# Kernel optimization log

Hardware: AMD Instinct MI355X
Metric: run time of the kernel (lower is better)

Reference implementation:

```python
import jax, jax.numpy as jnp
import numpy as np


def setup_inputs() -> dict:
    key = jax.random.key(0)
    ks = jax.random.split(key, 7)
    B, T, D, H = 32, 512, 512, 512
    return {
        "x": jax.random.normal(ks[0], (B, T, D), dtype=jnp.float32),
        "W_Du": jax.random.normal(ks[1], (D, H), dtype=jnp.float32) * (1.0 / np.sqrt(D)),
        "W_Dr1": jax.random.normal(ks[2], (D, H), dtype=jnp.float32) * (1.0 / np.sqrt(D)),
        "W_Dr2": jax.random.normal(ks[3], (D, H), dtype=jnp.float32) * (1.0 / np.sqrt(D)),
        "b_Du": jax.random.normal(ks[4], (H,), dtype=jnp.float32) * 0.02,
        "b_Dr1": jax.random.normal(ks[5], (H,), dtype=jnp.float32) * 0.02,
        "b_Dr2": jax.random.normal(ks[6], (H,), dtype=jnp.float32) * 0.02,
    }


def reference(x, W_Du, W_Dr1, W_Dr2, b_Du, b_Dr1, b_Dr2):
    # Precompute all per-step projections across time (batched matmuls),
    # then run the strictly sequential gated recurrence with lax.scan.
    r1 = jax.nn.softmax(jnp.einsum('btd,dh->bth', x, W_Dr1) + b_Dr1, axis=-1)  # [B,T,H]
    r2 = jax.nn.softmax(jnp.einsum('btd,dh->bth', x, W_Dr2) + b_Dr2, axis=-1)  # [B,T,H]
    u = jnp.tanh(jnp.einsum('btd,dh->bth', x, W_Du) + b_Du)                     # [B,T,H]

    def step(s, inp):
        r1t, r2t, ut = inp
        s_new = r1t * s + r2t * ut
        return s_new, s_new

    init = jnp.zeros((x.shape[0], W_Du.shape[1]), dtype=x.dtype)
    # time-major for scan: [T,B,H]
    _, ys = jax.lax.scan(
        step, init,
        (jnp.swapaxes(r1, 0, 1), jnp.swapaxes(r2, 0, 1), jnp.swapaxes(u, 0, 1)),
    )
    return jnp.swapaxes(ys, 0, 1)  # [B,T,H]
```

## Files before the change

### kernel.cpp

```cpp
#include <hip/hip_runtime.h>
#include <hip/hip_bf16.h>

#define B_N 32
#define T_N 512
#define D_N 512
#define H_N 512
#define M_N (B_N * T_N)

typedef __attribute__((ext_vector_type(8))) short bf16x8;
typedef __attribute__((ext_vector_type(4))) float f32x4;

__device__ __forceinline__ unsigned short f2bf(float f) {
  unsigned u = __float_as_uint(f);
  u += 0x7FFFu + ((u >> 16) & 1u);
  return (unsigned short)(u >> 16);
}
__device__ __forceinline__ float bf2f(unsigned short h) {
  return __uint_as_float(((unsigned)h) << 16);
}
__device__ __forceinline__ unsigned short f2h(float f) {
  _Float16 h = (_Float16)f;
  return *(unsigned short*)&h;
}
__device__ __forceinline__ float h2f(unsigned short u) {
  _Float16 h = *(_Float16*)&u;
  return (float)h;
}

#define GLOAD16(g, l) __builtin_amdgcn_global_load_lds( \
    (const __attribute__((address_space(1))) void*)(g), \
    (__attribute__((address_space(3))) void*)(l), 16, 0, 0)

__global__ void prep_kernel(const float* __restrict__ x,
                            const float* __restrict__ W0,
                            const float* __restrict__ W1,
                            const float* __restrict__ W2,
                            unsigned short* __restrict__ xb,
                            unsigned short* __restrict__ Wt) {
  int blk = blockIdx.x;
  int tid = threadIdx.x;
  if (blk < 768) {
    __shared__ float tile[32][33];
    int id = blk >> 8;
    int t = blk & 255;
    int kr = (t >> 4) << 5;
    int nc = (t & 15) << 5;
    const float* W = (id == 0) ? W0 : (id == 1) ? W1 : W2;
    unsigned short* Wo = Wt + (size_t)id * (D_N * H_N);
    int tx = tid & 31, ty0 = tid >> 5;
    for (int ty = ty0; ty < 32; ty += 8)
      tile[ty][tx] = W[(size_t)(kr + ty) * H_N + nc + tx];
    __syncthreads();
    for (int ty = ty0; ty < 32; ty += 8)
      Wo[(size_t)(nc + ty) * D_N + kr + tx] = f2bf(tile[tx][ty]);
  } else {
    int b = blk - 768;
    const float4* xv = (const float4*)x;
#pragma unroll
    for (int u = 0; u < 4; ++u) {
      int i = b * 1024 + u * 256 + tid;
      float4 v = xv[i];
      ushort4 o;
      o.x = f2bf(v.x); o.y = f2bf(v.y); o.z = f2bf(v.z); o.w = f2bf(v.w);
      ((ushort4*)xb)[i] = o;
    }
  }
}

__global__ __launch_bounds__(256) void gemm3(
    const unsigned short* __restrict__ xb,
    const unsigned short* __restrict__ Wt,
    const float* __restrict__ bDu,
    const float* __restrict__ bDr1,
    const float* __restrict__ bDr2,
    unsigned short* __restrict__ uP,
    unsigned short* __restrict__ e1P,
    unsigned short* __restrict__ e2P) {
  __shared__ __align__(16) char smem[65536];

  const int tid = threadIdx.x;
  const int lane = tid & 63;
  const int wv = tid >> 6;
  const int wr = wv >> 1;
  const int wc = wv & 1;
  const int g = lane >> 4;
  const int c16 = lane & 15;

  const int m0 = blockIdx.x * 128;
  const int n0 = blockIdx.y * 128;
  const int id = blockIdx.z;
  const unsigned short* Wp = Wt + (size_t)id * (D_N * H_N);

  f32x4 acc[4][4];
#pragma unroll
  for (int mt = 0; mt < 4; ++mt)
#pragma unroll
    for (int nt = 0; nt < 4; ++nt)
      acc[mt][nt] = (f32x4){0.f, 0.f, 0.f, 0.f};

  const int rowoff = tid >> 3;
  const int lsl = ((tid & 7) ^ ((tid >> 3) & 7)) * 8;
  const unsigned short* aSrc = xb + (size_t)(m0 + rowoff) * D_N + lsl;
  const unsigned short* bSrc = Wp + (size_t)(n0 + rowoff) * D_N + lsl;
  const int dstOff = wv * 1024;

  const int h3 = c16 & 7;

#define STAGE(buf, kstep) do {                                           \
    const int k0_ = (kstep) * 64;                                        \
    _Pragma("unroll")                                                    \
    for (int i = 0; i < 4; ++i)                                          \
      GLOAD16(aSrc + (size_t)i * (32 * D_N) + k0_,                       \
              smem + (buf) * 16384 + dstOff + i * 4096);                 \
    _Pragma("unroll")                                                    \
    for (int i = 0; i < 4; ++i)                                          \
      GLOAD16(bSrc + (size_t)i * (32 * D_N) + k0_,                       \
              smem + 32768 + (buf) * 16384 + dstOff + i * 4096);         \
  } while (0)

#define COMPUTE(buf) do {                                                \
    _Pragma("unroll")                                                    \
    for (int kh = 0; kh < 2; ++kh) {                                     \
      const int soff = ((kh * 4 + g) ^ h3) << 4;                         \
      bf16x8 af[4], bb[4];                                               \
      _Pragma("unroll")                                                  \
      for (int mt = 0; mt < 4; ++mt)                                     \
        af[mt] = *(const bf16x8*)(smem + (buf) * 16384 +                 \
                                  (wr * 64 + mt * 16 + c16) * 128 + soff); \
      _Pragma("unroll")                                                  \
      for (int nt = 0; nt < 4; ++nt)                                     \
        bb[nt] = *(const bf16x8*)(smem + 32768 + (buf) * 16384 +         \
                                  (wc * 64 + nt * 16 + c16) * 128 + soff); \
      _Pragma("unroll")                                                  \
      for (int mt = 0; mt < 4; ++mt)                                     \
        _Pragma("unroll")                                                \
        for (int nt = 0; nt < 4; ++nt)                                   \
          acc[mt][nt] = __builtin_amdgcn_mfma_f32_16x16x32_bf16(         \
              af[mt], bb[nt], acc[mt][nt], 0, 0, 0);                     \
    }                                                                    \
  } while (0)

#define WAIT8 asm volatile("s_waitcnt vmcnt(8)" ::: "memory")

  STAGE(0, 0);
#pragma unroll 1
  for (int i = 0; i < 3; ++i) {
    STAGE(1, 2 * i + 1);
    WAIT8;
    __syncthreads();
    COMPUTE(0);
    __syncthreads();
    STAGE(0, 2 * i + 2);
    WAIT8;
    __syncthreads();
    COMPUTE(1);
    __syncthreads();
  }
  STAGE(1, 7);
  WAIT8;
  __syncthreads();
  COMPUTE(0);
  __syncthreads();
  asm volatile("s_waitcnt vmcnt(0)" ::: "memory");
  __syncthreads();
  COMPUTE(1);

  const float* bp = (id == 0) ? bDu : (id == 1) ? bDr1 : bDr2;
  unsigned short* outp = (id == 0) ? uP : (id == 1) ? e1P : e2P;
  float bias[4];
#pragma unroll
  for (int nt = 0; nt < 4; ++nt)
    bias[nt] = bp[n0 + wc * 64 + nt * 16 + c16];

#pragma unroll
  for (int mt = 0; mt < 4; ++mt)
#pragma unroll
    for (int i = 0; i < 4; ++i) {
      int row = m0 + wr * 64 + mt * 16 + g * 4 + i;
      unsigned short* op = outp + (size_t)row * H_N + n0 + wc * 64 + c16;
      if (id == 0) {
#pragma unroll
        for (int nt = 0; nt < 4; ++nt) {
          float z = acc[mt][nt][i] + bias[nt];
          float e = __expf(2.f * z);
          op[nt * 16] = f2h(1.f - 2.f * __builtin_amdgcn_rcpf(e + 1.f));
        }
      } else {
#pragma unroll
        for (int nt = 0; nt < 4; ++nt)
          op[nt * 16] = f2h(__expf(acc[mt][nt][i] + bias[nt]));
      }
    }
#undef STAGE
#undef COMPUTE
#undef WAIT8
}

__global__ void rowsum(const unsigned short* __restrict__ e1P,
                       const unsigned short* __restrict__ e2P,
                       float* __restrict__ iS1,
                       float* __restrict__ iS2) {
  int row = blockIdx.x * 4 + (threadIdx.x >> 6);
  int lane = threadIdx.x & 63;
  const bf16x8 v1 = *(const bf16x8*)(e1P + (size_t)row * H_N + lane * 8);
  const bf16x8 v2 = *(const bf16x8*)(e2P + (size_t)row * H_N + lane * 8);
  float s1 = 0.f, s2 = 0.f;
#pragma unroll
  for (int i = 0; i < 8; ++i) {
    s1 += h2f((unsigned short)v1[i]);
    s2 += h2f((unsigned short)v2[i]);
  }
#pragma unroll
  for (int d = 1; d < 64; d <<= 1) {
    s1 += __shfl_xor(s1, d);
    s2 += __shfl_xor(s2, d);
  }
  if (lane == 0) {
    iS1[row] = 1.f / s1;
    iS2[row] = 1.f / s2;
  }
}

__global__ void scan_pass1(const unsigned short* __restrict__ e1P,
                           const unsigned short* __restrict__ e2P,
                           const unsigned short* __restrict__ uP,
                           const float* __restrict__ iS1,
                           const float* __restrict__ iS2,
                           float* __restrict__ cP,
                           float* __restrict__ cS) {
  int gt = blockIdx.x * 256 + threadIdx.x;
  int chunk = gt >> 14;
  int r = gt & 16383;
  int b = r >> 9, h = r & 511;
  int row0 = b * T_N + chunk * 64;
  size_t idx = (size_t)row0 * H_N + h;
  float p = 1.f, s = 0.f;
#pragma unroll 4
  for (int j = 0; j < 64; ++j) {
    float a = iS1[row0 + j] * h2f(e1P[idx]);
    float cu = iS2[row0 + j] * h2f(e2P[idx]) * h2f(uP[idx]);
    s = fmaf(a, s, cu);
    p *= a;
    idx += H_N;
  }
  cP[gt] = p;
  cS[gt] = s;
}

__global__ void scan_pass3(const unsigned short* __restrict__ e1P,
                           const unsigned short* __restrict__ e2P,
                           const unsigned short* __restrict__ uP,
                           const float* __restrict__ iS1,
                           const float* __restrict__ iS2,
                           const float* __restrict__ cP,
                           const float* __restrict__ cS,
                           float* __restrict__ out) {
  int gt = blockIdx.x * 256 + threadIdx.x;
  int chunk = gt >> 14;
  int r = gt & 16383;
  int b = r >> 9, h = r & 511;
  float s = 0.f;
  for (int c2 = 0; c2 < chunk; ++c2)
    s = fmaf(cP[c2 * 16384 + r], s, cS[c2 * 16384 + r]);
  int row0 = b * T_N + chunk * 64;
  size_t idx = (size_t)row0 * H_N + h;
#pragma unroll 4
  for (int j = 0; j < 64; ++j) {
    float a = iS1[row0 + j] * h2f(e1P[idx]);
    float cu = iS2[row0 + j] * h2f(e2P[idx]) * h2f(uP[idx]);
    s = fmaf(a, s, cu);
    out[idx] = s;
    idx += H_N;
  }
}

extern "C" void kernel_launch(void* const* d_in, const int* in_sizes, int n_in,
                              void* d_out, int out_size, void* d_ws, size_t ws_size,
                              hipStream_t stream) {
  const float* x  = (const float*)d_in[0];
  const float* W0 = (const float*)d_in[1];
  const float* W1 = (const float*)d_in[2];
  const float* W2 = (const float*)d_in[3];
  const float* b0 = (const float*)d_in[4];
  const float* b1 = (const float*)d_in[5];
  const float* b2 = (const float*)d_in[6];
  float* out = (float*)d_out;

  char* ws = (char*)d_ws;
  unsigned short* xb  = (unsigned short*)ws;
  unsigned short* Wt  = (unsigned short*)(ws + 16777216);
  unsigned short* uP  = (unsigned short*)(ws + 18350080);
  unsigned short* e1P = (unsigned short*)(ws + 35127296);
  unsigned short* e2P = (unsigned short*)(ws + 51904512);
  float*          iS1 = (float*)(ws + 68681728);
  float*          iS2 = (float*)(ws + 68747264);
  float*          cP  = (float*)(ws + 68812800);
  float*          cS  = (float*)(ws + 69337088);

  prep_kernel<<<2816, 256, 0, stream>>>(x, W0, W1, W2, xb, Wt);
  gemm3<<<dim3(128, 4, 3), 256, 0, stream>>>(xb, Wt, b0, b1, b2, uP, e1P, e2P);
  rowsum<<<4096, 256, 0, stream>>>(e1P, e2P, iS1, iS2);
  scan_pass1<<<512, 256, 0, stream>>>(e1P, e2P, uP, iS1, iS2, cP, cS);
  scan_pass3<<<512, 256, 0, stream>>>(e1P, e2P, uP, iS1, iS2, cP, cS, out);
}
```

Before: 83.11 us.

## Fuse softmax row sums into GEMM epilogue and triple-buffer K=32 stages

The separate rowsum pass that reread both exp tensors is replaced by a per-row partial sum in the GEMM epilogue. Each block reduces its partial sum across lanes and adds it atomically into a zeroed buffer, which a tiny kernel then inverts. The GEMM main loop also moves from double-buffered 64-wide K steps to triple-buffered 32-wide steps, with one combined waitcnt and barrier per step and less shared memory. The changes remove a full read of two large intermediates but add atomics, two extra tiny launches and an unswizzled LDS layout that may cause bank conflicts.

```diff
diff --git a/kernel.cpp b/kernel.cpp
--- a/kernel.cpp
+++ b/kernel.cpp
@@ -14,9 +14,6 @@
   unsigned u = __float_as_uint(f);
   u += 0x7FFFu + ((u >> 16) & 1u);
   return (unsigned short)(u >> 16);
-}
-__device__ __forceinline__ float bf2f(unsigned short h) {
-  return __uint_as_float(((unsigned)h) << 16);
 }
 __device__ __forceinline__ unsigned short f2h(float f) {
   _Float16 h = (_Float16)f;
@@ -67,6 +64,15 @@
   }
 }
 
+__global__ void zero_sums(float* __restrict__ S) {
+  ((float4*)S)[blockIdx.x * 256 + threadIdx.x] = (float4){0.f, 0.f, 0.f, 0.f};
+}
+
+__global__ void inv_sums(float* __restrict__ S) {
+  int i = blockIdx.x * 256 + threadIdx.x;
+  S[i] = 1.f / S[i];
+}
+
 __global__ __launch_bounds__(256) void gemm3(
     const unsigned short* __restrict__ xb,
     const unsigned short* __restrict__ Wt,
@@ -75,8 +81,10 @@
     const float* __restrict__ bDr2,
     unsigned short* __restrict__ uP,
     unsigned short* __restrict__ e1P,
-    unsigned short* __restrict__ e2P) {
-  __shared__ __align__(16) char smem[65536];
+    unsigned short* __restrict__ e2P,
+    float* __restrict__ S1,
+    float* __restrict__ S2) {
+  __shared__ __align__(16) char smem[49152];
 
   const int tid = threadIdx.x;
   const int lane = tid & 63;
@@ -98,75 +106,60 @@
     for (int nt = 0; nt < 4; ++nt)
       acc[mt][nt] = (f32x4){0.f, 0.f, 0.f, 0.f};
 
-  const int rowoff = tid >> 3;
-  const int lsl = ((tid & 7) ^ ((tid >> 3) & 7)) * 8;
-  const unsigned short* aSrc = xb + (size_t)(m0 + rowoff) * D_N + lsl;
-  const unsigned short* bSrc = Wp + (size_t)(n0 + rowoff) * D_N + lsl;
+  const int srow = wv * 16 + (lane >> 2);
+  const int selem = (lane & 3) * 8;
+  const unsigned short* aSrc = xb + (size_t)(m0 + srow) * D_N + selem;
+  const unsigned short* bSrc = Wp + (size_t)(n0 + srow) * D_N + selem;
   const int dstOff = wv * 1024;
 
-  const int h3 = c16 & 7;
-
-#define STAGE(buf, kstep) do {                                           \
-    const int k0_ = (kstep) * 64;                                        \
+#define STAGE(ab, kstep) do {                                            \
+    const int k0_ = (kstep) * 32;                                        \
+    GLOAD16(aSrc + k0_,                 smem + (ab) * 8192 + dstOff);    \
+    GLOAD16(aSrc + 64 * D_N + k0_,      smem + (ab) * 8192 + dstOff + 4096); \
+    GLOAD16(bSrc + k0_,         smem + 24576 + (ab) * 8192 + dstOff);    \
+    GLOAD16(bSrc + 64 * D_N + k0_, smem + 24576 + (ab) * 8192 + dstOff + 4096); \
+  } while (0)
+
+#define COMPUTE(ab) do {                                                 \
+    bf16x8 af[4], bb[4];                                                 \
     _Pragma("unroll")                                                    \
-    for (int i = 0; i < 4; ++i)                                          \
-      GLOAD16(aSrc + (size_t)i * (32 * D_N) + k0_,                       \
-              smem + (buf) * 16384 + dstOff + i * 4096);                 \
+    for (int mt = 0; mt < 4; ++mt)                                       \
+      af[mt] = *(const bf16x8*)(smem + (ab) * 8192 +                     \
+                                (wr * 64 + mt * 16 + c16) * 64 + g * 16); \
     _Pragma("unroll")                                                    \
-    for (int i = 0; i < 4; ++i)                                          \
-      GLOAD16(bSrc + (size_t)i * (32 * D_N) + k0_,                       \
-              smem + 32768 + (buf) * 16384 + dstOff + i * 4096);         \
-  } while (0)
-
-#define COMPUTE(buf) do {                                                \
+    for (int nt = 0; nt < 4; ++nt)                                       \
+      bb[nt] = *(const bf16x8*)(smem + 24576 + (ab) * 8192 +             \
+                                (wc * 64 + nt * 16 + c16) * 64 + g * 16); \
     _Pragma("unroll")                                                    \
-    for (int kh = 0; kh < 2; ++kh) {                                     \
-      const int soff = ((kh * 4 + g) ^ h3) << 4;                         \
-      bf16x8 af[4], bb[4];                                               \
-      _Pragma("unroll")                                                  \
-      for (int mt = 0; mt < 4; ++mt)                                     \
-        af[mt] = *(const bf16x8*)(smem + (buf) * 16384 +                 \
-                                  (wr * 64 + mt * 16 + c16) * 128 + soff); \
+    for (int mt = 0; mt < 4; ++mt)                                       \
       _Pragma("unroll")                                                  \
       for (int nt = 0; nt < 4; ++nt)                                     \
-        bb[nt] = *(const bf16x8*)(smem + 32768 + (buf) * 16384 +         \
-                                  (wc * 64 + nt * 16 + c16) * 128 + soff); \
-      _Pragma("unroll")                                                  \
-      for (int mt = 0; mt < 4; ++mt)                                     \
-        _Pragma("unroll")                                                \
-        for (int nt = 0; nt < 4; ++nt)                                   \
-          acc[mt][nt] = __builtin_amdgcn_mfma_f32_16x16x32_bf16(         \
-              af[mt], bb[nt], acc[mt][nt], 0, 0, 0);                     \
-    }                                                                    \
+        acc[mt][nt] = __builtin_amdgcn_mfma_f32_16x16x32_bf16(           \
+            af[mt], bb[nt], acc[mt][nt], 0, 0, 0);                       \
   } while (0)
 
-#define WAIT8 asm volatile("s_waitcnt vmcnt(8)" ::: "memory")
+#define WB(n) do {                                                       \
+    __builtin_amdgcn_sched_barrier(0);                                   \
+    asm volatile("s_waitcnt vmcnt(" #n ")\n\ts_barrier" ::: "memory");   \
+    __builtin_amdgcn_sched_barrier(0);                                   \
+  } while (0)
 
   STAGE(0, 0);
+  STAGE(1, 1);
 #pragma unroll 1
-  for (int i = 0; i < 3; ++i) {
-    STAGE(1, 2 * i + 1);
-    WAIT8;
-    __syncthreads();
-    COMPUTE(0);
-    __syncthreads();
-    STAGE(0, 2 * i + 2);
-    WAIT8;
-    __syncthreads();
-    COMPUTE(1);
-    __syncthreads();
-  }
-  STAGE(1, 7);
-  WAIT8;
-  __syncthreads();
-  COMPUTE(0);
-  __syncthreads();
-  asm volatile("s_waitcnt vmcnt(0)" ::: "memory");
-  __syncthreads();
-  COMPUTE(1);
+  for (int i = 0; i < 4; ++i) {
+    WB(4); STAGE(2, 3 * i + 2); COMPUTE(0);
+    WB(4); STAGE(0, 3 * i + 3); COMPUTE(1);
+    WB(4); STAGE(1, 3 * i + 4); COMPUTE(2);
+  }
+  WB(4); STAGE(2, 14); COMPUTE(0);
+  WB(4); STAGE(0, 15); COMPUTE(1);
+  WB(4); COMPUTE(2);
+  WB(0); COMPUTE(0);
 
   const float* bp = (id == 0) ? bDu : (id == 1) ? bDr1 : bDr2;
   unsigned short* outp = (id == 0) ? uP : (id == 1) ? e1P : e2P;
+  float* Sp = (id == 1) ? S1 : S2;
   float bias[4];
 #pragma unroll
   for (int nt = 0; nt < 4; ++nt)
@@ -186,39 +179,23 @@
           op[nt * 16] = f2h(1.f - 2.f * __builtin_amdgcn_rcpf(e + 1.f));
         }
       } else {
-#pragma unroll
-        for (int nt = 0; nt < 4; ++nt)
-          op[nt * 16] = f2h(__expf(acc[mt][nt][i] + bias[nt]));
+        float ps = 0.f;
+#pragma unroll
+        for (int nt = 0; nt < 4; ++nt) {
+          float e = __expf(acc[mt][nt][i] + bias[nt]);
+          op[nt * 16] = f2h(e);
+          ps += e;
+        }
+        ps += __shfl_xor(ps, 1);
+        ps += __shfl_xor(ps, 2);
+        ps += __shfl_xor(ps, 4);
+        ps += __shfl_xor(ps, 8);
+        if (c16 == 0) atomicAdd(&Sp[row], ps);
       }
     }
 #undef STAGE
 #undef COMPUTE
-#undef WAIT8
-}
-
-__global__ void rowsum(const unsigned short* __restrict__ e1P,
-                       const unsigned short* __restrict__ e2P,
-                       float* __restrict__ iS1,
-                       float* __restrict__ iS2) {
-  int row = blockIdx.x * 4 + (threadIdx.x >> 6);
-  int lane = threadIdx.x & 63;
-  const bf16x8 v1 = *(const bf16x8*)(e1P + (size_t)row * H_N + lane * 8);
-  const bf16x8 v2 = *(const bf16x8*)(e2P + (size_t)row * H_N + lane * 8);
-  float s1 = 0.f, s2 = 0.f;
-#pragma unroll
-  for (int i = 0; i < 8; ++i) {
-    s1 += h2f((unsigned short)v1[i]);
-    s2 += h2f((unsigned short)v2[i]);
-  }
-#pragma unroll
-  for (int d = 1; d < 64; d <<= 1) {
-    s1 += __shfl_xor(s1, d);
-    s2 += __shfl_xor(s2, d);
-  }
-  if (lane == 0) {
-    iS1[row] = 1.f / s1;
-    iS2[row] = 1.f / s2;
-  }
+#undef WB
 }
 
 __global__ void scan_pass1(const unsigned short* __restrict__ e1P,
@@ -292,14 +269,16 @@
   unsigned short* uP  = (unsigned short*)(ws + 18350080);
   unsigned short* e1P = (unsigned short*)(ws + 35127296);
   unsigned short* e2P = (unsigned short*)(ws + 51904512);
-  float*          iS1 = (float*)(ws + 68681728);
-  float*          iS2 = (float*)(ws + 68747264);
+  float*          S1  = (float*)(ws + 68681728);
+  float*          S2  = (float*)(ws + 68747264);
   float*          cP  = (float*)(ws + 68812800);
   float*          cS  = (float*)(ws + 69337088);
 
+  zero_sums<<<32, 256, 0, stream>>>(S1);
   prep_kernel<<<2816, 256, 0, stream>>>(x, W0, W1, W2, xb, Wt);
-  gemm3<<<dim3(128, 4, 3), 256, 0, stream>>>(xb, Wt, b0, b1, b2, uP, e1P, e2P);
-  rowsum<<<4096, 256, 0, stream>>>(e1P, e2P, iS1, iS2);
-  scan_pass1<<<512, 256, 0, stream>>>(e1P, e2P, uP, iS1, iS2, cP, cS);
-  scan_pass3<<<512, 256, 0, stream>>>(e1P, e2P, uP, iS1, iS2, cP, cS, out);
-}
+  gemm3<<<dim3(128, 4, 3), 256, 0, stream>>>(xb, Wt, b0, b1, b2,
+                                             uP, e1P, e2P, S1, S2);
+  inv_sums<<<128, 256, 0, stream>>>(S1);
+  scan_pass1<<<512, 256, 0, stream>>>(e1P, e2P, uP, S1, S2, cP, cS);
+  scan_pass3<<<512, 256, 0, stream>>>(e1P, e2P, uP, S1, S2, cP, cS, out);
+}
```

Measured after the change: 90.78 us. +9.2%, slower.
